# Performance work log

Hardware: AMD Instinct MI355X
Metric: run time of the kernel (lower is better)

The kernel has to match this reference:

```python
import jax, jax.numpy as jnp
import numpy as np
from jax import lax

EPSILON = 1e-4

def _sobel_kernels(dtype=jnp.float32):
    kx = jnp.array([[1., 0., -1.], [2., 0., -2.], [1., 0., -1.]], dtype=dtype)[None, None] / 4.0
    ky = jnp.array([[1., 2., 1.], [0., 0., 0.], [-1., -2., -1.]], dtype=dtype)[None, None] / 4.0
    return kx, ky


def setup_inputs() -> dict:
    key = jax.random.key(0)
    x = jax.random.normal(key, (64, 1, 512, 512), dtype=jnp.float32)
    return {"x": x}


def reference(x) -> jnp.ndarray:
    # x: [B, 1, H, W]; two depthwise-style 3x3 convs (single channel), padding=1,
    # then fused magnitude: sqrt(gx^2 + gy^2 + eps)
    kx, ky = _sobel_kernels(x.dtype)
    dn = lax.conv_dimension_numbers(x.shape, kx.shape, ("NCHW", "OIHW", "NCHW"))
    conv = lambda k: lax.conv_general_dilated(x, k, window_strides=(1, 1),
                                              padding=((1, 1), (1, 1)),
                                              dimension_numbers=dn)
    grad_x = conv(kx)
    grad_y = conv(ky)
    return jnp.sqrt(grad_x * grad_x + grad_y * grad_y + EPSILON)
```

## Files before the change

kernel.cpp:

```cpp
#include <hip/hip_runtime.h>
#include <math.h>

#define IMG_W 512
#define IMG_H 512
#define TILE_ROWS 16
#define ROWS_PT 8
#define EPS16 1.6e-3f

struct RowWin {
    float l;
    float m0, m1, m2, m3;
    float r;
};

__device__ __forceinline__ RowWin load_row(const float* __restrict__ img,
                                           int r, int cf) {
    RowWin w;
    if (r < 0 || r >= IMG_H) {
        w.l = w.m0 = w.m1 = w.m2 = w.m3 = w.r = 0.f;
        return w;
    }
    const float* p = img + (size_t)r * IMG_W + 4 * cf;
    float4 v = *reinterpret_cast<const float4*>(p);
    w.m0 = v.x; w.m1 = v.y; w.m2 = v.z; w.m3 = v.w;
    w.l = (cf > 0)              ? p[-1] : 0.f;
    w.r = (cf < IMG_W / 4 - 1)  ? p[4]  : 0.f;
    return w;
}

__global__ __launch_bounds__(256) void sobel_kernel(const float* __restrict__ x,
                                                    float* __restrict__ out) {
    const int tid  = threadIdx.x;
    const int cf   = tid & 127;
    const int half = tid >> 7;
    const int r0   = blockIdx.x * TILE_ROWS + half * ROWS_PT;

    const float* img = x   + (size_t)blockIdx.y * (IMG_H * IMG_W);
    float*       o   = out + (size_t)blockIdx.y * (IMG_H * IMG_W);

    RowWin A = load_row(img, r0 - 1, cf);
    RowWin B = load_row(img, r0,     cf);

    for (int i = 0; i < ROWS_PT; ++i) {
        const int r = r0 + i;
        RowWin C = load_row(img, r + 1, cf);

        float sl = A.l  + 2.f * B.l  + C.l;
        float s0 = A.m0 + 2.f * B.m0 + C.m0;
        float s1 = A.m1 + 2.f * B.m1 + C.m1;
        float s2 = A.m2 + 2.f * B.m2 + C.m2;
        float s3 = A.m3 + 2.f * B.m3 + C.m3;
        float sr = A.r  + 2.f * B.r  + C.r;

        float dl = A.l  - C.l;
        float d0 = A.m0 - C.m0;
        float d1 = A.m1 - C.m1;
        float d2 = A.m2 - C.m2;
        float d3 = A.m3 - C.m3;
        float dr = A.r  - C.r;

        float gx0 = sl - s1, gx1 = s0 - s2, gx2 = s1 - s3, gx3 = s2 - sr;
        float gy0 = dl + 2.f * d0 + d1;
        float gy1 = d0 + 2.f * d1 + d2;
        float gy2 = d1 + 2.f * d2 + d3;
        float gy3 = d2 + 2.f * d3 + dr;

        float4 res;
        res.x = 0.25f * sqrtf(gx0 * gx0 + gy0 * gy0 + EPS16);
        res.y = 0.25f * sqrtf(gx1 * gx1 + gy1 * gy1 + EPS16);
        res.z = 0.25f * sqrtf(gx2 * gx2 + gy2 * gy2 + EPS16);
        res.w = 0.25f * sqrtf(gx3 * gx3 + gy3 * gy3 + EPS16);

        *reinterpret_cast<float4*>(o + (size_t)r * IMG_W + 4 * cf) = res;

        A = B; B = C;
    }
}

extern "C" void kernel_launch(void* const* d_in, const int* in_sizes, int n_in,
                              void* d_out, int out_size, void* d_ws, size_t ws_size,
                              hipStream_t stream) {
    const float* x = (const float*)d_in[0];
    float* out = (float*)d_out;
    const int batch = in_sizes[0] / (IMG_H * IMG_W);
    dim3 grid(IMG_H / TILE_ROWS, batch);
    sobel_kernel<<<grid, 256, 0, stream>>>(x, out);
}
```

Measured before the change: 119.0 us.

## Map one wavefront per row and fetch halo columns via cross-lane shuffles

Each 64-lane wavefront now covers a full 512-wide row as two float4 segments per lane. Left and right halo values come from lane shuffles instead of extra scalar global loads, and the segment boundaries at columns 255/256 are stitched with broadcast shuffles. Each block covers 32 rows with four waves instead of 16, which halves the number of blocks, and the row loop is fully unrolled. This removes the redundant unaligned scalar loads per row but adds shuffle instructions and register pressure.

```diff
diff --git a/kernel.cpp b/kernel.cpp
--- a/kernel.cpp
+++ b/kernel.cpp
@@ -3,75 +3,93 @@
 
 #define IMG_W 512
 #define IMG_H 512
-#define TILE_ROWS 16
 #define ROWS_PT 8
+#define WAVES_PER_BLOCK 4
+#define TILE_ROWS (ROWS_PT * WAVES_PER_BLOCK)
 #define EPS16 1.6e-3f
 
-struct RowWin {
-    float l;
-    float m0, m1, m2, m3;
-    float r;
+struct Row {
+    float4 a;
+    float4 b;
+    float la, ra, lb, rb;
 };
 
-__device__ __forceinline__ RowWin load_row(const float* __restrict__ img,
-                                           int r, int cf) {
-    RowWin w;
+__device__ __forceinline__ Row load_row(const float* __restrict__ img, int r, int lane) {
+    Row w;
     if (r < 0 || r >= IMG_H) {
-        w.l = w.m0 = w.m1 = w.m2 = w.m3 = w.r = 0.f;
+        w.a = make_float4(0.f, 0.f, 0.f, 0.f);
+        w.b = make_float4(0.f, 0.f, 0.f, 0.f);
+        w.la = w.ra = w.lb = w.rb = 0.f;
         return w;
     }
-    const float* p = img + (size_t)r * IMG_W + 4 * cf;
-    float4 v = *reinterpret_cast<const float4*>(p);
-    w.m0 = v.x; w.m1 = v.y; w.m2 = v.z; w.m3 = v.w;
-    w.l = (cf > 0)              ? p[-1] : 0.f;
-    w.r = (cf < IMG_W / 4 - 1)  ? p[4]  : 0.f;
+    const float* p = img + (size_t)r * IMG_W + 4 * lane;
+    w.a = *reinterpret_cast<const float4*>(p);
+    w.b = *reinterpret_cast<const float4*>(p + 256);
+    float c255 = __shfl(w.a.w, 63);
+    float c256 = __shfl(w.b.x, 0);
+    w.la = __shfl_up(w.a.w, 1);
+    w.ra = __shfl_down(w.a.x, 1);
+    w.lb = __shfl_up(w.b.w, 1);
+    w.rb = __shfl_down(w.b.x, 1);
+    if (lane == 0)  { w.la = 0.f;  w.lb = c255; }
+    if (lane == 63) { w.ra = c256; w.rb = 0.f;  }
     return w;
+}
+
+__device__ __forceinline__ float4 sobel_half(const float4& A, float Al, float Ar,
+                                             const float4& B, float Bl, float Br,
+                                             const float4& C, float Cl, float Cr) {
+    float sl = Al  + 2.f * Bl  + Cl;
+    float s0 = A.x + 2.f * B.x + C.x;
+    float s1 = A.y + 2.f * B.y + C.y;
+    float s2 = A.z + 2.f * B.z + C.z;
+    float s3 = A.w + 2.f * B.w + C.w;
+    float sr = Ar  + 2.f * Br  + Cr;
+
+    float dl = Al  - Cl;
+    float d0 = A.x - C.x;
+    float d1 = A.y - C.y;
+    float d2 = A.z - C.z;
+    float d3 = A.w - C.w;
+    float dr = Ar  - Cr;
+
+    float gx0 = sl - s1, gx1 = s0 - s2, gx2 = s1 - s3, gx3 = s2 - sr;
+    float gy0 = dl + 2.f * d0 + d1;
+    float gy1 = d0 + 2.f * d1 + d2;
+    float gy2 = d1 + 2.f * d2 + d3;
+    float gy3 = d2 + 2.f * d3 + dr;
+
+    float4 res;
+    res.x = 0.25f * sqrtf(gx0 * gx0 + gy0 * gy0 + EPS16);
+    res.y = 0.25f * sqrtf(gx1 * gx1 + gy1 * gy1 + EPS16);
+    res.z = 0.25f * sqrtf(gx2 * gx2 + gy2 * gy2 + EPS16);
+    res.w = 0.25f * sqrtf(gx3 * gx3 + gy3 * gy3 + EPS16);
+    return res;
 }
 
 __global__ __launch_bounds__(256) void sobel_kernel(const float* __restrict__ x,
                                                     float* __restrict__ out) {
-    const int tid  = threadIdx.x;
-    const int cf   = tid & 127;
-    const int half = tid >> 7;
-    const int r0   = blockIdx.x * TILE_ROWS + half * ROWS_PT;
+    const int lane = threadIdx.x & 63;
+    const int wave = threadIdx.x >> 6;
+    const int r0   = blockIdx.x * TILE_ROWS + wave * ROWS_PT;
 
     const float* img = x   + (size_t)blockIdx.y * (IMG_H * IMG_W);
     float*       o   = out + (size_t)blockIdx.y * (IMG_H * IMG_W);
 
-    RowWin A = load_row(img, r0 - 1, cf);
-    RowWin B = load_row(img, r0,     cf);
+    Row A = load_row(img, r0 - 1, lane);
+    Row B = load_row(img, r0,     lane);
 
+#pragma unroll
     for (int i = 0; i < ROWS_PT; ++i) {
         const int r = r0 + i;
-        RowWin C = load_row(img, r + 1, cf);
+        Row C = load_row(img, r + 1, lane);
 
-        float sl = A.l  + 2.f * B.l  + C.l;
-        float s0 = A.m0 + 2.f * B.m0 + C.m0;
-        float s1 = A.m1 + 2.f * B.m1 + C.m1;
-        float s2 = A.m2 + 2.f * B.m2 + C.m2;
-        float s3 = A.m3 + 2.f * B.m3 + C.m3;
-        float sr = A.r  + 2.f * B.r  + C.r;
+        float4 ra = sobel_half(A.a, A.la, A.ra, B.a, B.la, B.ra, C.a, C.la, C.ra);
+        float4 rb = sobel_half(A.b, A.lb, A.rb, B.b, B.lb, B.rb, C.b, C.lb, C.rb);
 
-        float dl = A.l  - C.l;
-        float d0 = A.m0 - C.m0;
-        float d1 = A.m1 - C.m1;
-        float d2 = A.m2 - C.m2;
-        float d3 = A.m3 - C.m3;
-        float dr = A.r  - C.r;
-
-        float gx0 = sl - s1, gx1 = s0 - s2, gx2 = s1 - s3, gx3 = s2 - sr;
-        float gy0 = dl + 2.f * d0 + d1;
-        float gy1 = d0 + 2.f * d1 + d2;
-        float gy2 = d1 + 2.f * d2 + d3;
-        float gy3 = d2 + 2.f * d3 + dr;
-
-        float4 res;
-        res.x = 0.25f * sqrtf(gx0 * gx0 + gy0 * gy0 + EPS16);
-        res.y = 0.25f * sqrtf(gx1 * gx1 + gy1 * gy1 + EPS16);
-        res.z = 0.25f * sqrtf(gx2 * gx2 + gy2 * gy2 + EPS16);
-        res.w = 0.25f * sqrtf(gx3 * gx3 + gy3 * gy3 + EPS16);
-
-        *reinterpret_cast<float4*>(o + (size_t)r * IMG_W + 4 * cf) = res;
+        float* po = o + (size_t)r * IMG_W + 4 * lane;
+        *reinterpret_cast<float4*>(po)       = ra;
+        *reinterpret_cast<float4*>(po + 256) = rb;
 
         A = B; B = C;
     }
```

Measured after the change: 113.6 us. 4.5% less time.
